# Performance work log

Hardware: AMD Instinct MI355X
Metric: run time of the kernel (lower is better)

## Reference

```python
import jax, jax.numpy as jnp
import numpy as np
from jax import lax

EPS = 1e-5
H = 4      # num_heads
D = 64     # qkv_dim (== in_channels)


def _bn(x, gamma, beta, mean, var):
    # eval-mode BatchNorm2d over NCHW, channel axis 1
    inv = gamma / jnp.sqrt(var + EPS)
    return x * inv[:, None, None] + (beta - mean * inv)[:, None, None]


def _conv(x, w, b, pad_w):
    y = lax.conv_general_dilated(x, w, window_strides=(1, 1),
                                 padding=[(0, 0), (pad_w, pad_w)],
                                 dimension_numbers=("NCHW", "OIHW", "NCHW"))
    return y + b[None, :, None, None]


def setup_inputs() -> dict:
    key = jax.random.key(0)
    ks = jax.random.split(key, 16)
    N, C, T, V = 16, 64, 64, 25
    s = 0.05
    return {
        "x": jax.random.normal(ks[0], (N, C, T, V), jnp.float32),
        "W_qkv": jax.random.normal(ks[1], (C, 3 * H * D), jnp.float32) * s,
        "b_qkv": jax.random.normal(ks[2], (3 * H * D,), jnp.float32) * s,
        "W_out": jax.random.normal(ks[3], (C, C * H, 1, 9), jnp.float32) * s,
        "b_out": jax.random.normal(ks[4], (C,), jnp.float32) * s,
        "bn1_gamma": jax.random.uniform(ks[5], (C,), jnp.float32) + 0.5,
        "bn1_beta": jax.random.normal(ks[6], (C,), jnp.float32) * s,
        "bn1_mean": jax.random.normal(ks[7], (C,), jnp.float32) * s,
        "bn1_var": jax.random.uniform(ks[8], (C,), jnp.float32) + 0.5,
        "W_ff": jax.random.normal(ks[9], (C, C, 1, 1), jnp.float32) * s,
        "b_ff": jax.random.normal(ks[10], (C,), jnp.float32) * s,
        "bn2_gamma": jax.random.uniform(ks[11], (C,), jnp.float32) + 0.5,
        "bn2_beta": jax.random.normal(ks[12], (C,), jnp.float32) * s,
        "bn2_mean": jax.random.normal(ks[13], (C,), jnp.float32) * s,
        "bn2_var": jax.random.uniform(ks[14], (C,), jnp.float32) + 0.5,
    }


def reference(x, W_qkv, b_qkv, W_out, b_out, bn1_gamma, bn1_beta, bn1_mean,
              bn1_var, W_ff, b_ff, bn2_gamma, bn2_beta, bn2_mean, bn2_var):
    N, C, T, V = x.shape
    L = T * V
    # qkv projection on [N,T,V,C]
    xt = jnp.transpose(x, (0, 2, 3, 1))                        # [N,T,V,C]
    qkv = xt.reshape(N, L, C) @ W_qkv + b_qkv                  # [N,L,3*H*D]
    qkv = qkv.reshape(N, L, 3, H, D)
    q = jnp.transpose(qkv[:, :, 0], (0, 2, 1, 3))              # [N,H,L,D]
    k = jnp.transpose(qkv[:, :, 1], (0, 2, 1, 3))              # [N,H,L,D]
    v = jnp.transpose(qkv[:, :, 2], (0, 2, 1, 3))              # [N,H,L,D]
    attn = jnp.einsum("nhld,nhmd->nhlm", q, k) / jnp.sqrt(jnp.float32(D))
    attn = jax.nn.softmax(attn, axis=-1)
    o = jnp.einsum("nhlm,nhmd->nhld", attn, v)                 # [N,H,L,D]
    # view(N,H,T,V,D).permute(0,1,4,2,3).view(N,H*D,T,V)
    o = o.reshape(N, H, T, V, D)
    o = jnp.transpose(o, (0, 1, 4, 2, 3)).reshape(N, H * D, T, V)
    # out_nets: Conv2d (1,9) pad (0,4) + BN, residual (identity), relu
    y = _bn(_conv(o, W_out, b_out, 4), bn1_gamma, bn1_beta, bn1_mean, bn1_var)
    y = jax.nn.relu(y + x)
    # ff_net: 1x1 conv + BN, residual, relu
    z = _bn(_conv(y, W_ff, b_ff, 0), bn2_gamma, bn2_beta, bn2_mean, bn2_var)
    return jax.nn.relu(z + y)
```

## Files before the change

kernel.cpp:

```cpp
#include <hip/hip_runtime.h>
#include <hip/hip_bf16.h>

#define NB 16
#define CC 64
#define TT 64
#define VV 25
#define LL 1600
#define HH 4
#define DD 64
#define NH 64


typedef __hip_bfloat16 bf16;
typedef __attribute__((ext_vector_type(8))) short short8;
typedef __attribute__((ext_vector_type(4))) float f32x4;
typedef __attribute__((ext_vector_type(4))) int int4v;
typedef __attribute__((ext_vector_type(4))) unsigned short us4;

__device__ __forceinline__ float b2f(bf16 v) { return __bfloat162float(v); }
__device__ __forceinline__ unsigned short f2bf_bits(float f) {
  bf16 h = __float2bfloat16(f);
  return *(unsigned short*)&h;
}
__device__ __forceinline__ unsigned pkbf_trunc(float lo, float hi) {
  return __builtin_amdgcn_perm(__float_as_uint(hi), __float_as_uint(lo), 0x07060302u);
}
__device__ __forceinline__ float dppx1(float x) {
  return __int_as_float(
      __builtin_amdgcn_mov_dpp(__float_as_int(x), 0xB1, 0xF, 0xF, true));
}
__device__ __forceinline__ int dppx1i(int x) {
  return __builtin_amdgcn_mov_dpp(x, 0xB1, 0xF, 0xF, true);
}
__device__ __forceinline__ void pl32swap(int &a, int &b) {
  asm("v_permlane32_swap_b32 %0, %1" : "+v"(a), "+v"(b));
}
__device__ __forceinline__ void pl16swap(int &a, int &b) {
  asm("v_permlane16_swap_b32 %0, %1" : "+v"(a), "+v"(b));
}

__global__ void k_prep(const float* __restrict__ Wo, const float* __restrict__ Wf,
                       const float* __restrict__ Wq,
                       bf16* __restrict__ Wt, bf16* __restrict__ WfT,
                       bf16* __restrict__ WqT) {
  int i = blockIdx.x * 256 + threadIdx.x;
  if (i < 147456) {
    int j = i & 7, lane = (i >> 3) & 63, cot = (i >> 9) & 3;
    int kc = (i >> 11) & 7, r = i >> 14;
    int co = cot * 16 + (lane & 15);
    int ci = kc * 32 + (lane >> 4) * 8 + j;
    Wt[i] = __float2bfloat16(Wo[(co * 256 + ci) * 9 + r]);
  }
  if (i < 4096) {
    int j = i & 7, lane = (i >> 3) & 63, cot = (i >> 9) & 3, kc = (i >> 11) & 1;
    int co = cot * 16 + (lane & 15);
    int ci = kc * 32 + (lane >> 4) * 8 + j;
    WfT[i] = __float2bfloat16(Wf[co * 64 + ci]);
  }
  if (i < 49152) {
    int jj = i & 7, lane = (i >> 3) & 63, g = i >> 9;
    int nt = g % 48, half = g / 48;
    int ch = half * 32 + (lane >> 4) * 8 + jj;
    int j = nt * 16 + (lane & 15);
    WqT[i] = __float2bfloat16(Wq[ch * 768 + j]);
  }
}

__global__ __launch_bounds__(256)
void k_qkv(const float* __restrict__ x, const bf16* __restrict__ WqT,
           const float* __restrict__ bq,
           bf16* __restrict__ q, bf16* __restrict__ k, bf16* __restrict__ vt) {
  __shared__ short xa_all[4][16 * 72];
  __shared__ short tr_all[4][16 * 66];
  int tid = threadIdx.x;
  int wv = tid >> 6, lane = tid & 63;
  int quad = lane >> 4, c = lane & 15;
  int g4 = blockIdx.x * 4 + wv;
  int n = g4 / 100;
  int l0 = (g4 % 100) * 16;
  short* xa = xa_all[wv];
  short* tr = tr_all[wv];
  bool ev = (c & 1) == 0;

  {
    int l = c;
    const float* xb = x + (size_t)n * 102400 + (size_t)(quad * 16) * 1600 + l0 + l;
    unsigned short vb[16];
#pragma unroll
    for (int i = 0; i < 16; i++) vb[i] = f2bf_bits(xb[(size_t)i * 1600]);
    unsigned wrds[8];
#pragma unroll
    for (int i = 0; i < 8; i++)
      wrds[i] = ((unsigned)vb[2 * i + 1] << 16) | vb[2 * i];
    *(short8*)(xa + l * 72 + quad * 16) = *(short8*)&wrds[0];
    *(short8*)(xa + l * 72 + quad * 16 + 8) = *(short8*)&wrds[4];
  }
  asm volatile("" ::: "memory");
  short8 af0 = *(const short8*)(xa + c * 72 + quad * 8);
  short8 af1 = *(const short8*)(xa + c * 72 + 32 + quad * 8);

  const short* wq0 = (const short*)WqT;
  const float QSCALE = 0.125f * 1.44269504f;

  short8 bc[8], bn[8];
#pragma unroll
  for (int t = 0; t < 4; t++) {
    bc[2 * t]     = *(const short8*)(wq0 + ((size_t)t * 64 + lane) * 8);
    bc[2 * t + 1] = *(const short8*)(wq0 + ((size_t)(48 + t) * 64 + lane) * 8);
  }

#pragma unroll
  for (int g = 0; g < 12; g++) {
    int s = g >> 2, h = g & 3;
    f32x4 z[4];
#pragma unroll
    for (int t = 0; t < 4; t++) {
      int nt = g * 4 + t;
      float bv = bq[nt * 16 + c];
      f32x4 zz = {bv, bv, bv, bv};
      zz = __builtin_amdgcn_mfma_f32_16x16x32_bf16(af0, bc[2 * t], zz, 0, 0, 0);
      zz = __builtin_amdgcn_mfma_f32_16x16x32_bf16(af1, bc[2 * t + 1], zz, 0, 0, 0);
      z[t] = zz;
    }
    if (g < 11) {
#pragma unroll
      for (int t = 0; t < 4; t++) {
        int nt = (g + 1) * 4 + t;
        bn[2 * t]     = *(const short8*)(wq0 + ((size_t)nt * 64 + lane) * 8);
        bn[2 * t + 1] = *(const short8*)(wq0 + ((size_t)(48 + nt) * 64 + lane) * 8);
      }
    }
    if (s < 2) {
      asm volatile("" ::: "memory");
#pragma unroll
      for (int t = 0; t < 4; t++) {
        if (s == 0) {
#pragma unroll
          for (int r = 0; r < 4; r++) z[t][r] *= QSCALE;
        }
        int us_[4];
#pragma unroll
        for (int r = 0; r < 4; r++) us_[r] = f2bf_bits(z[t][r]);
        int xv0 = dppx1i(us_[0]);
        int xv1 = dppx1i(us_[1]);
        int xv2 = dppx1i(us_[2]);
        int xv3 = dppx1i(us_[3]);
        if (ev) {
          *(int*)(tr + (quad * 4 + 0) * 66 + t * 16 + c) = (xv0 << 16) | us_[0];
          *(int*)(tr + (quad * 4 + 1) * 66 + t * 16 + c) = (xv1 << 16) | us_[1];
        } else {
          *(int*)(tr + (quad * 4 + 2) * 66 + t * 16 + (c - 1)) = (us_[2] << 16) | xv2;
          *(int*)(tr + (quad * 4 + 3) * 66 + t * 16 + (c - 1)) = (us_[3] << 16) | xv3;
        }
      }
      asm volatile("" ::: "memory");
      int row = lane >> 2, seg = lane & 3;
      short8 o0 = *(const short8*)(tr + row * 66 + seg * 16);
      short8 o1 = *(const short8*)(tr + row * 66 + seg * 16 + 8);
      short* dstp = (short*)(s == 0 ? q : k);
      short* dst = dstp + ((size_t)(n * 4 + h) * 1600 + l0 + row) * 64 + seg * 16;
      *(short8*)(dst) = o0;
      *(short8*)(dst + 8) = o1;
      asm volatile("" ::: "memory");
    } else {
#pragma unroll
      for (int t = 0; t < 4; t++) {
        us4 pk;
#pragma unroll
        for (int r = 0; r < 4; r++) pk[r] = f2bf_bits(z[t][r]);
        *(us4*)((short*)vt + ((size_t)((n * 4 + h) * 64 + t * 16 + c)) * 1600 +
                l0 + quad * 4) = pk;
      }
    }
#pragma unroll
    for (int i = 0; i < 8; i++) bc[i] = bn[i];
  }
}

__global__ __launch_bounds__(256, 2)
void k_attn(const bf16* __restrict__ q, const bf16* __restrict__ k,
            const bf16* __restrict__ vt, bf16* __restrict__ po,
            float* __restrict__ ls, int split) {
  __shared__ short kbuf[64 * 64];
  __shared__ short vbuf[64 * 64];
  __shared__ short pl_all[4][16 * 66];
  int tid = threadIdx.x;
  int wv = tid >> 6, lane = tid & 63;
  int quad = lane >> 4, c = lane & 15;
  int bid = blockIdx.x;
  int xcd = bid & 7;
  int slot = bid >> 3;
  int half, qt, grp;
  if (split == 2) { half = slot & 1; qt = (slot >> 1) % 25; grp = slot / 50; }
  else            { half = 0;        qt = slot % 25;        grp = slot / 25; }
  int nh = grp * 8 + xcd;
  int kt0 = half ? 13 : 0;
  int kt1 = (split == 2 && half == 0) ? 13 : 25;
  int l0 = qt * 64 + wv * 16;
  short* pl = pl_all[wv];

  const short* qbase = (const short*)q + ((size_t)nh * 1600 + l0 + c) * 64 + quad * 8;
  short8 qf0 = *(const short8*)(qbase);
  short8 qf1 = *(const short8*)(qbase + 32);

  short ob = (c == 0) ? (short)0x3F80 : (short)0;
  short8 onesf = {ob, ob, ob, ob, ob, ob, ob, ob};

  f32x4 acc[5] = {};

  const short* kg = (const short*)k + (size_t)nh * 102400;
  const short* vg = (const short*)vt + (size_t)nh * 102400;
  bool ev = (c & 1) == 0;

  int wrow = tid >> 3;
  int wseg0 = (tid & 7) ^ (wrow & 7);
  int wseg1 = (tid & 7) ^ ((wrow + 32) & 7);
  int cx = c & 7;
  int rseg0 = quad ^ cx;
  int rseg1 = (quad + 4) ^ cx;

  short8 sk[2], sv[2];
  {
    const short8* gk = (const short8*)(kg + kt0 * 4096);
#pragma unroll
    for (int i = 0; i < 2; i++) sk[i] = gk[tid + i * 256];
#pragma unroll
    for (int i = 0; i < 2; i++) {
      int ch = tid + i * 256;
      sv[i] = *(const short8*)(vg + (size_t)(ch >> 3) * 1600 + kt0 * 64 + (ch & 7) * 8);
    }
  }

  for (int kt = kt0; kt < kt1; kt++) {
    __syncthreads();
#pragma unroll
    for (int i = 0; i < 2; i++) {
      int row = wrow + i * 32;
      int seg = (i == 0) ? wseg0 : wseg1;
      *(short8*)(kbuf + row * 64 + seg * 8) = sk[i];
      *(short8*)(vbuf + row * 64 + seg * 8) = sv[i];
    }
    __syncthreads();
    if (kt + 1 < kt1) {
      const short8* gk = (const short8*)(kg + (kt + 1) * 4096);
#pragma unroll
      for (int i = 0; i < 2; i++) sk[i] = gk[tid + i * 256];
#pragma unroll
      for (int i = 0; i < 2; i++) {
        int ch = tid + i * 256;
        sv[i] = *(const short8*)(vg + (size_t)(ch >> 3) * 1600 + (kt + 1) * 64 + (ch & 7) * 8);
      }
    }
    f32x4 s[4];
#pragma unroll
    for (int ct = 0; ct < 4; ct++) {
      const short* kr = kbuf + (ct * 16 + c) * 64;
      short8 kf0 = *(const short8*)(kr + rseg0 * 8);
      short8 kf1 = *(const short8*)(kr + rseg1 * 8);
      f32x4 z0 = {-8.f, -8.f, -8.f, -8.f};
      z0 = __builtin_amdgcn_mfma_f32_16x16x32_bf16(kf0, qf0, z0, 0, 0, 0);
      z0 = __builtin_amdgcn_mfma_f32_16x16x32_bf16(kf1, qf1, z0, 0, 0, 0);
      s[ct] = z0;
    }
#pragma unroll
    for (int ct = 0; ct < 4; ct++)
#pragma unroll
      for (int r = 0; r < 4; r++) s[ct][r] = exp2f(s[ct][r]);
    short8 vf[4][2];
#pragma unroll
    for (int ct = 0; ct < 4; ct++) {
      const short* vr = vbuf + (ct * 16 + c) * 64;
      vf[ct][0] = *(const short8*)(vr + rseg0 * 8);
      vf[ct][1] = *(const short8*)(vr + rseg1 * 8);
    }
    {
      int wA[4], wB[4];
#pragma unroll
      for (int ct = 0; ct < 4; ct++) {
        wA[ct] = (int)pkbf_trunc(s[ct][0], s[ct][1]);
        wB[ct] = (int)pkbf_trunc(s[ct][2], s[ct][3]);
      }
      pl32swap(wA[0], wA[1]); pl16swap(wA[0], wA[1]);
      pl32swap(wB[0], wB[1]); pl16swap(wB[0], wB[1]);
      int4v f0 = {wA[0], wB[0], wA[1], wB[1]};
      pl32swap(wA[2], wA[3]); pl16swap(wA[2], wA[3]);
      pl32swap(wB[2], wB[3]); pl16swap(wB[2], wB[3]);
      int4v f1 = {wA[2], wB[2], wA[3], wB[3]};
      short8 pf0 = *(short8*)&f0;
      short8 pf1 = *(short8*)&f1;
#pragma unroll
      for (int ct = 0; ct < 4; ct++) {
        acc[ct] = __builtin_amdgcn_mfma_f32_16x16x32_bf16(pf0, vf[ct][0], acc[ct], 0, 0, 0);
        acc[ct] = __builtin_amdgcn_mfma_f32_16x16x32_bf16(pf1, vf[ct][1], acc[ct], 0, 0, 0);
      }
      acc[4] = __builtin_amdgcn_mfma_f32_16x16x32_bf16(pf0, onesf, acc[4], 0, 0, 0);
      acc[4] = __builtin_amdgcn_mfma_f32_16x16x32_bf16(pf1, onesf, acc[4], 0, 0, 0);
    }
  }
  int n = nh >> 2, h = nh & 3;
  {
    float linv[4] = {1.f, 1.f, 1.f, 1.f};
    if (split == 1) {
#pragma unroll
      for (int r = 0; r < 4; r++)
        linv[r] = 1.0f / __shfl(acc[4][r], lane & 48);
    }
    asm volatile("" ::: "memory");
#pragma unroll
    for (int t = 0; t < 4; t++) {
      int us_[4];
#pragma unroll
      for (int r = 0; r < 4; r++) us_[r] = f2bf_bits(acc[t][r] * linv[r]);
      int xv0 = dppx1i(us_[0]);
      int xv1 = dppx1i(us_[1]);
      int xv2 = dppx1i(us_[2]);
      int xv3 = dppx1i(us_[3]);
      if (ev) {
        *(int*)(pl + (quad * 4 + 0) * 66 + t * 16 + c) = (xv0 << 16) | us_[0];
        *(int*)(pl + (quad * 4 + 1) * 66 + t * 16 + c) = (xv1 << 16) | us_[1];
      } else {
        *(int*)(pl + (quad * 4 + 2) * 66 + t * 16 + (c - 1)) = (us_[2] << 16) | xv2;
        *(int*)(pl + (quad * 4 + 3) * 66 + t * 16 + (c - 1)) = (us_[3] << 16) | xv3;
      }
    }
    asm volatile("" ::: "memory");
    int row = lane >> 2, seg = lane & 3;
    short8 o0 = *(const short8*)(pl + row * 66 + seg * 16);
    short8 o1 = *(const short8*)(pl + row * 66 + seg * 16 + 8);
    short* dst = (short*)po + (size_t)half * 6553600 +
                 ((size_t)n * 1600 + l0 + row) * 256 + h * 64 + seg * 16;
    *(short8*)(dst) = o0;
    *(short8*)(dst + 8) = o1;
    if (split == 2 && c == 0) {
#pragma unroll
      for (int r = 0; r < 4; r++)
        ls[half * 102400 + nh * 1600 + l0 + quad * 4 + r] = acc[4][r];
    }
    asm volatile("" ::: "memory");
  }
}

__global__ void k_comb(const bf16* po_in, const float* __restrict__ ls, bf16* ot) {
  int i = blockIdx.x * 256 + threadIdx.x;
  int ch8 = i & 31;
  int rest = i >> 5;
  int l = rest % 1600;
  int n = rest / 1600;
  int nh = n * 4 + (ch8 >> 3);
  float inv = 1.0f / (ls[nh * 1600 + l] + ls[102400 + nh * 1600 + l]);
  const short* a = (const short*)po_in + (size_t)rest * 256 + ch8 * 8;
  short8 av = *(const short8*)a;
  short8 bv = *(const short8*)(a + 6553600);
  unsigned short o8[8];
#pragma unroll
  for (int j = 0; j < 8; j++) {
    float fa = __uint_as_float(((unsigned)(unsigned short)av[j]) << 16);
    float fb = __uint_as_float(((unsigned)(unsigned short)bv[j]) << 16);
    o8[j] = f2bf_bits((fa + fb) * inv);
  }
  *(short8*)((short*)ot + (size_t)rest * 256 + ch8 * 8) = *(short8*)o8;
}

__global__ __launch_bounds__(256)
void k_conv9(const bf16* __restrict__ ot, const bf16* __restrict__ Wt,
             const float* __restrict__ bo, const float* __restrict__ g1,
             const float* __restrict__ be1, const float* __restrict__ mu1,
             const float* __restrict__ va1, const float* __restrict__ x,
             const bf16* __restrict__ WfT, const float* __restrict__ bff,
             const float* __restrict__ g2, const float* __restrict__ be2,
             const float* __restrict__ mu2, const float* __restrict__ va2,
             float* __restrict__ out) {
  __shared__ short tl[4][16 * 66];
  int tid = threadIdx.x;
  int wv = tid >> 6;
  int lane = tid & 63;
  int quad = lane >> 4, c = lane & 15;
  int n = blockIdx.y;
  int l0 = blockIdx.x * 64 + wv * 16;
  int la = l0 + c;
  int va = la % 25;
  const short* obase = (const short*)ot + (size_t)n * 409600;
  const short* wbase = (const short*)Wt;
  f32x4 acc[4] = {};
  for (int r = 0; r < 9; r++) {
    int sh = r - 4;
    bool valid = (unsigned)(va + sh) < 25u;
    int lp = la + sh;
    lp = max(0, min(1599, lp));
    const short* arow = obase + (size_t)lp * 256 + quad * 8;
    const short* wrow = wbase + (size_t)r * 8 * 4 * 64 * 8 + lane * 8;
    short8 z8 = {0, 0, 0, 0, 0, 0, 0, 0};
#pragma unroll 4
    for (int kc = 0; kc < 8; kc++) {
      short8 af = *(const short8*)(arow + kc * 32);
      af = valid ? af : z8;
      const short* wk = wrow + kc * 4 * 64 * 8;
      short8 b0 = *(const short8*)(wk);
      short8 b1 = *(const short8*)(wk + 512);
      short8 b2 = *(const short8*)(wk + 1024);
      short8 b3 = *(const short8*)(wk + 1536);
      acc[0] = __builtin_amdgcn_mfma_f32_16x16x32_bf16(af, b0, acc[0], 0, 0, 0);
      acc[1] = __builtin_amdgcn_mfma_f32_16x16x32_bf16(af, b1, acc[1], 0, 0, 0);
      acc[2] = __builtin_amdgcn_mfma_f32_16x16x32_bf16(af, b2, acc[2], 0, 0, 0);
      acc[3] = __builtin_amdgcn_mfma_f32_16x16x32_bf16(af, b3, acc[3], 0, 0, 0);
    }
  }
  short* tlw = &tl[wv][0];
  float outv[4][4];
#pragma unroll
  for (int cot = 0; cot < 4; cot++) {
    int co = cot * 16 + c;
    float inv = g1[co] * rsqrtf(va1[co] + 1e-5f);
    float add = be1[co] - mu1[co] * inv + bo[co] * inv;
    f32x4 xr = *(const f32x4*)(x + (size_t)(n * 64 + co) * 1600 + l0 + quad * 4);
#pragma unroll
    for (int rr = 0; rr < 4; rr++)
      outv[cot][rr] = fmaxf(acc[cot][rr] * inv + add + xr[rr], 0.f);
  }
  asm volatile("" ::: "memory");
  bool ev = (c & 1) == 0;
#pragma unroll
  for (int cot = 0; cot < 4; cot++) {
    int us_[4];
#pragma unroll
    for (int rr = 0; rr < 4; rr++) us_[rr] = f2bf_bits(outv[cot][rr]);
    int xv0 = dppx1i(us_[0]);
    int xv1 = dppx1i(us_[1]);
    int xv2 = dppx1i(us_[2]);
    int xv3 = dppx1i(us_[3]);
    if (ev) {
      *(int*)(tlw + (quad * 4 + 0) * 66 + cot * 16 + c) = (xv0 << 16) | us_[0];
      *(int*)(tlw + (quad * 4 + 1) * 66 + cot * 16 + c) = (xv1 << 16) | us_[1];
    } else {
      *(int*)(tlw + (quad * 4 + 2) * 66 + cot * 16 + (c - 1)) = (us_[2] << 16) | xv2;
      *(int*)(tlw + (quad * 4 + 3) * 66 + cot * 16 + (c - 1)) = (us_[3] << 16) | xv3;
    }
  }
  asm volatile("" ::: "memory");
  short8 afY0 = *(const short8*)(tlw + c * 66 + quad * 8);
  short8 afY1 = *(const short8*)(tlw + c * 66 + 32 + quad * 8);
  const short* wfb = (const short*)WfT + lane * 8;
  f32x4 acc2[4] = {};
#pragma unroll
  for (int kc = 0; kc < 2; kc++) {
    short8 afk = kc ? afY1 : afY0;
    const short* wk = wfb + kc * 2048;
    short8 b0 = *(const short8*)(wk);
    short8 b1 = *(const short8*)(wk + 512);
    short8 b2 = *(const short8*)(wk + 1024);
    short8 b3 = *(const short8*)(wk + 1536);
    acc2[0] = __builtin_amdgcn_mfma_f32_16x16x32_bf16(afk, b0, acc2[0], 0, 0, 0);
    acc2[1] = __builtin_amdgcn_mfma_f32_16x16x32_bf16(afk, b1, acc2[1], 0, 0, 0);
    acc2[2] = __builtin_amdgcn_mfma_f32_16x16x32_bf16(afk, b2, acc2[2], 0, 0, 0);
    acc2[3] = __builtin_amdgcn_mfma_f32_16x16x32_bf16(afk, b3, acc2[3], 0, 0, 0);
  }
#pragma unroll
  for (int cot = 0; cot < 4; cot++) {
    int co = cot * 16 + c;
    float inv = g2[co] * rsqrtf(va2[co] + 1e-5f);
    float add = be2[co] - mu2[co] * inv + bff[co] * inv;
    f32x4 ov;
#pragma unroll
    for (int rr = 0; rr < 4; rr++)
      ov[rr] = fmaxf(acc2[cot][rr] * inv + add + outv[cot][rr], 0.f);
    *(f32x4*)(out + (size_t)(n * 64 + co) * 1600 + l0 + quad * 4) = ov;
  }
}

extern "C" void kernel_launch(void* const* d_in, const int* in_sizes, int n_in,
                              void* d_out, int out_size, void* d_ws, size_t ws_size,
                              hipStream_t stream) {
  const float* x   = (const float*)d_in[0];
  const float* Wq  = (const float*)d_in[1];
  const float* bq  = (const float*)d_in[2];
  const float* Wo  = (const float*)d_in[3];
  const float* bo  = (const float*)d_in[4];
  const float* g1  = (const float*)d_in[5];
  const float* be1 = (const float*)d_in[6];
  const float* mu1 = (const float*)d_in[7];
  const float* va1 = (const float*)d_in[8];
  const float* Wf  = (const float*)d_in[9];
  const float* bff = (const float*)d_in[10];
  const float* g2  = (const float*)d_in[11];
  const float* be2 = (const float*)d_in[12];
  const float* mu2 = (const float*)d_in[13];
  const float* va2 = (const float*)d_in[14];

  const size_t QKV = (size_t)64 * 1600 * 64;
  size_t elems2 = 5 * QKV + 147456 + 4096 + 49152;
  size_t need2 = elems2 * 2 + 2 * 102400 * 4 + 256;
  int split = (ws_size >= need2) ? 2 : 1;

  bf16* qw  = (bf16*)d_ws;
  bf16* kw  = qw + QKV;
  bf16* vtw = kw + QKV;
  bf16* pow_ = vtw + QKV;
  bf16* Wt  = pow_ + (size_t)split * QKV;
  bf16* WfT = Wt + 147456;
  bf16* WqT = WfT + 4096;
  float* ls = (float*)(WqT + 49152);

  k_prep<<<576, 256, 0, stream>>>(Wo, Wf, Wq, Wt, WfT, WqT);
  k_qkv<<<400, 256, 0, stream>>>(x, WqT, bq, qw, kw, vtw);
  k_attn<<<split * 1600, 256, 0, stream>>>(qw, kw, vtw, pow_, ls, split);
  if (split == 2) k_comb<<<3200, 256, 0, stream>>>(pow_, ls, pow_);
  dim3 gc(25, 16);
  k_conv9<<<gc, 256, 0, stream>>>(pow_, Wt, bo, g1, be1, mu1, va1, x,
                                  WfT, bff, g2, be2, mu2, va2, (float*)d_out);
}
```

Baseline: 216.7 us.

## Drop split-K attention and combine kernel; fold weight prep into attention grid

Removes the two-way split over key tiles in the attention kernel, along with the separate kernel that merged the partial outputs and row sums. Each block now processes all 25 key tiles and normalises by the softmax denominator in its epilogue. The conv9 and 1x1 weight reformatting moves out of the prep kernel into 576 extra trailing blocks of the attention launch, so the standalone prep kernel only converts Wq. This saves one launch and the partial-output round trip through memory. In exchange there are fewer, longer attention blocks, which could leave a worse tail across the CUs.

```diff
diff --git a/kernel.cpp b/kernel.cpp
--- a/kernel.cpp
+++ b/kernel.cpp
@@ -39,31 +39,13 @@
   asm("v_permlane16_swap_b32 %0, %1" : "+v"(a), "+v"(b));
 }
 
-__global__ void k_prep(const float* __restrict__ Wo, const float* __restrict__ Wf,
-                       const float* __restrict__ Wq,
-                       bf16* __restrict__ Wt, bf16* __restrict__ WfT,
-                       bf16* __restrict__ WqT) {
+__global__ void k_prep_wq(const float* __restrict__ Wq, bf16* __restrict__ WqT) {
   int i = blockIdx.x * 256 + threadIdx.x;
-  if (i < 147456) {
-    int j = i & 7, lane = (i >> 3) & 63, cot = (i >> 9) & 3;
-    int kc = (i >> 11) & 7, r = i >> 14;
-    int co = cot * 16 + (lane & 15);
-    int ci = kc * 32 + (lane >> 4) * 8 + j;
-    Wt[i] = __float2bfloat16(Wo[(co * 256 + ci) * 9 + r]);
-  }
-  if (i < 4096) {
-    int j = i & 7, lane = (i >> 3) & 63, cot = (i >> 9) & 3, kc = (i >> 11) & 1;
-    int co = cot * 16 + (lane & 15);
-    int ci = kc * 32 + (lane >> 4) * 8 + j;
-    WfT[i] = __float2bfloat16(Wf[co * 64 + ci]);
-  }
-  if (i < 49152) {
-    int jj = i & 7, lane = (i >> 3) & 63, g = i >> 9;
-    int nt = g % 48, half = g / 48;
-    int ch = half * 32 + (lane >> 4) * 8 + jj;
-    int j = nt * 16 + (lane & 15);
-    WqT[i] = __float2bfloat16(Wq[ch * 768 + j]);
-  }
+  int jj = i & 7, lane = (i >> 3) & 63, g = i >> 9;
+  int nt = g % 48, half = g / 48;
+  int ch = half * 32 + (lane >> 4) * 8 + jj;
+  int j = nt * 16 + (lane & 15);
+  WqT[i] = __float2bfloat16(Wq[ch * 768 + j]);
 }
 
 __global__ __launch_bounds__(256)
@@ -180,22 +162,36 @@
 __global__ __launch_bounds__(256, 2)
 void k_attn(const bf16* __restrict__ q, const bf16* __restrict__ k,
             const bf16* __restrict__ vt, bf16* __restrict__ po,
-            float* __restrict__ ls, int split) {
+            const float* __restrict__ Wo, const float* __restrict__ Wf,
+            bf16* __restrict__ Wt, bf16* __restrict__ WfT) {
   __shared__ short kbuf[64 * 64];
   __shared__ short vbuf[64 * 64];
   __shared__ short pl_all[4][16 * 66];
   int tid = threadIdx.x;
+  int bid = blockIdx.x;
+  if (bid >= 1600) {
+    int i = (bid - 1600) * 256 + tid;
+    {
+      int j = i & 7, lane = (i >> 3) & 63, cot = (i >> 9) & 3;
+      int kc = (i >> 11) & 7, r = i >> 14;
+      int co = cot * 16 + (lane & 15);
+      int ci = kc * 32 + (lane >> 4) * 8 + j;
+      Wt[i] = __float2bfloat16(Wo[(co * 256 + ci) * 9 + r]);
+    }
+    if (i < 4096) {
+      int j = i & 7, lane = (i >> 3) & 63, cot = (i >> 9) & 3, kc = (i >> 11) & 1;
+      int co = cot * 16 + (lane & 15);
+      int ci = kc * 32 + (lane >> 4) * 8 + j;
+      WfT[i] = __float2bfloat16(Wf[co * 64 + ci]);
+    }
+    return;
+  }
   int wv = tid >> 6, lane = tid & 63;
   int quad = lane >> 4, c = lane & 15;
-  int bid = blockIdx.x;
   int xcd = bid & 7;
   int slot = bid >> 3;
-  int half, qt, grp;
-  if (split == 2) { half = slot & 1; qt = (slot >> 1) % 25; grp = slot / 50; }
-  else            { half = 0;        qt = slot % 25;        grp = slot / 25; }
+  int qt = slot % 25, grp = slot / 25;
   int nh = grp * 8 + xcd;
-  int kt0 = half ? 13 : 0;
-  int kt1 = (split == 2 && half == 0) ? 13 : 25;
   int l0 = qt * 64 + wv * 16;
   short* pl = pl_all[wv];
 
@@ -213,35 +209,33 @@
   bool ev = (c & 1) == 0;
 
   int wrow = tid >> 3;
-  int wseg0 = (tid & 7) ^ (wrow & 7);
-  int wseg1 = (tid & 7) ^ ((wrow + 32) & 7);
+  int wseg = (tid & 7) ^ (wrow & 7);
   int cx = c & 7;
   int rseg0 = quad ^ cx;
   int rseg1 = (quad + 4) ^ cx;
 
   short8 sk[2], sv[2];
   {
-    const short8* gk = (const short8*)(kg + kt0 * 4096);
+    const short8* gk = (const short8*)(kg);
 #pragma unroll
     for (int i = 0; i < 2; i++) sk[i] = gk[tid + i * 256];
 #pragma unroll
     for (int i = 0; i < 2; i++) {
       int ch = tid + i * 256;
-      sv[i] = *(const short8*)(vg + (size_t)(ch >> 3) * 1600 + kt0 * 64 + (ch & 7) * 8);
-    }
-  }
-
-  for (int kt = kt0; kt < kt1; kt++) {
+      sv[i] = *(const short8*)(vg + (size_t)(ch >> 3) * 1600 + (ch & 7) * 8);
+    }
+  }
+
+  for (int kt = 0; kt < 25; kt++) {
     __syncthreads();
 #pragma unroll
     for (int i = 0; i < 2; i++) {
       int row = wrow + i * 32;
-      int seg = (i == 0) ? wseg0 : wseg1;
-      *(short8*)(kbuf + row * 64 + seg * 8) = sk[i];
-      *(short8*)(vbuf + row * 64 + seg * 8) = sv[i];
+      *(short8*)(kbuf + row * 64 + wseg * 8) = sk[i];
+      *(short8*)(vbuf + row * 64 + wseg * 8) = sv[i];
     }
     __syncthreads();
-    if (kt + 1 < kt1) {
+    if (kt + 1 < 25) {
       const short8* gk = (const short8*)(kg + (kt + 1) * 4096);
 #pragma unroll
       for (int i = 0; i < 2; i++) sk[i] = gk[tid + i * 256];
@@ -299,12 +293,10 @@
   }
   int n = nh >> 2, h = nh & 3;
   {
-    float linv[4] = {1.f, 1.f, 1.f, 1.f};
-    if (split == 1) {
-#pragma unroll
-      for (int r = 0; r < 4; r++)
-        linv[r] = 1.0f / __shfl(acc[4][r], lane & 48);
-    }
+    float linv[4];
+#pragma unroll
+    for (int r = 0; r < 4; r++)
+      linv[r] = 1.0f / __shfl(acc[4][r], lane & 48);
     asm volatile("" ::: "memory");
 #pragma unroll
     for (int t = 0; t < 4; t++) {
@@ -327,38 +319,12 @@
     int row = lane >> 2, seg = lane & 3;
     short8 o0 = *(const short8*)(pl + row * 66 + seg * 16);
     short8 o1 = *(const short8*)(pl + row * 66 + seg * 16 + 8);
-    short* dst = (short*)po + (size_t)half * 6553600 +
+    short* dst = (short*)po +
                  ((size_t)n * 1600 + l0 + row) * 256 + h * 64 + seg * 16;
     *(short8*)(dst) = o0;
     *(short8*)(dst + 8) = o1;
-    if (split == 2 && c == 0) {
-#pragma unroll
-      for (int r = 0; r < 4; r++)
-        ls[half * 102400 + nh * 1600 + l0 + quad * 4 + r] = acc[4][r];
-    }
     asm volatile("" ::: "memory");
   }
-}
-
-__global__ void k_comb(const bf16* po_in, const float* __restrict__ ls, bf16* ot) {
-  int i = blockIdx.x * 256 + threadIdx.x;
-  int ch8 = i & 31;
-  int rest = i >> 5;
-  int l = rest % 1600;
-  int n = rest / 1600;
-  int nh = n * 4 + (ch8 >> 3);
-  float inv = 1.0f / (ls[nh * 1600 + l] + ls[102400 + nh * 1600 + l]);
-  const short* a = (const short*)po_in + (size_t)rest * 256 + ch8 * 8;
-  short8 av = *(const short8*)a;
-  short8 bv = *(const short8*)(a + 6553600);
-  unsigned short o8[8];
-#pragma unroll
-  for (int j = 0; j < 8; j++) {
-    float fa = __uint_as_float(((unsigned)(unsigned short)av[j]) << 16);
-    float fb = __uint_as_float(((unsigned)(unsigned short)bv[j]) << 16);
-    o8[j] = f2bf_bits((fa + fb) * inv);
-  }
-  *(short8*)((short*)ot + (size_t)rest * 256 + ch8 * 8) = *(short8*)o8;
 }
 
 __global__ __launch_bounds__(256)
@@ -487,23 +453,17 @@
   const float* va2 = (const float*)d_in[14];
 
   const size_t QKV = (size_t)64 * 1600 * 64;
-  size_t elems2 = 5 * QKV + 147456 + 4096 + 49152;
-  size_t need2 = elems2 * 2 + 2 * 102400 * 4 + 256;
-  int split = (ws_size >= need2) ? 2 : 1;
-
   bf16* qw  = (bf16*)d_ws;
   bf16* kw  = qw + QKV;
   bf16* vtw = kw + QKV;
   bf16* pow_ = vtw + QKV;
-  bf16* Wt  = pow_ + (size_t)split * QKV;
+  bf16* Wt  = pow_ + QKV;
   bf16* WfT = Wt + 147456;
   bf16* WqT = WfT + 4096;
-  float* ls = (float*)(WqT + 49152);
-
-  k_prep<<<576, 256, 0, stream>>>(Wo, Wf, Wq, Wt, WfT, WqT);
+
+  k_prep_wq<<<192, 256, 0, stream>>>(Wq, WqT);
   k_qkv<<<400, 256, 0, stream>>>(x, WqT, bq, qw, kw, vtw);
-  k_attn<<<split * 1600, 256, 0, stream>>>(qw, kw, vtw, pow_, ls, split);
-  if (split == 2) k_comb<<<3200, 256, 0, stream>>>(pow_, ls, pow_);
+  k_attn<<<1600 + 576, 256, 0, stream>>>(qw, kw, vtw, pow_, Wo, Wf, Wt, WfT);
   dim3 gc(25, 16);
   k_conv9<<<gc, 256, 0, stream>>>(pow_, Wt, bo, g1, be1, mu1, va1, x,
                                   WfT, bff, g2, be2, mu2, va2, (float*)d_out);
```

After: 215.2 us. About the same (-0.7%).
